# Kernel optimization log

Measured on AMD Instinct MI355X. Metric: run time of the kernel, lower is better.

The kernel has to match this reference:

```python
import jax, jax.numpy as jnp
import numpy as np

N_NODES = 100000
N_EDGES = 3200000


def setup_inputs() -> dict:
    key = jax.random.key(0)
    ks = jax.random.split(key, 8)
    n_in, h1, h2 = 512, 512, 128
    # xavier-uniform-ish scaling for weights
    lim1 = (6.0 / (n_in + h1)) ** 0.5
    lim2 = (6.0 / (h1 + h2)) ** 0.5
    return {
        "seq_a": jax.random.normal(ks[0], (N_NODES, n_in), dtype=jnp.float32),
        "W1": jax.random.uniform(ks[1], (n_in, h1), jnp.float32, -lim1, lim1),
        "b1": jnp.zeros((h1,), jnp.float32),
        "W2": jax.random.uniform(ks[2], (h1, h2), jnp.float32, -lim2, lim2),
        "b2": jnp.zeros((h2,), jnp.float32),
        "adj_rows": jnp.sort(jax.random.randint(ks[3], (N_EDGES,), 0, N_NODES, jnp.int32)),
        "adj_cols": jax.random.randint(ks[4], (N_EDGES,), 0, N_NODES, jnp.int32),
        "adj_vals": jax.random.uniform(ks[5], (N_EDGES,), jnp.float32),
    }


def reference(seq_a, W1, b1, W2, b2, adj_rows, adj_cols, adj_vals):
    # Eval-mode forward: F.dropout is identity when training=False.
    # MLP: Linear(n_in,512) + ReLU, Linear(512,128) (no activation on last layer)
    h = jax.nn.relu(seq_a @ W1 + b1)          # [N, 512]
    h_a = h @ W2 + b2                          # [N, 128]
    # Sparse aggregation: h_p = adj @ h_a with adj in COO form.
    # h_p[r] = sum over edges e with row r of vals[e] * h_a[cols[e]]
    msgs = adj_vals[:, None] * h_a[adj_cols]   # [E, 128] irregular gather
    h_p = jax.ops.segment_sum(msgs, adj_rows, num_segments=N_NODES)  # [N, 128]
    return (h_a, h_p)
```

## Files before the change

### kernel.cpp

```cpp
#include <hip/hip_runtime.h>

#define N_NODES 100000
#define ROWS_PAD 100096
#define NIN 512
#define H1  512
#define H2  128
#define N_EDGES 3200000

typedef __attribute__((ext_vector_type(8))) short bf16x8;
typedef __attribute__((ext_vector_type(4))) float f32x4;
typedef __attribute__((ext_vector_type(2))) float f32x2;

__device__ __forceinline__ unsigned short f2b(float x) {
  union { float f; unsigned int u; } c; c.f = x;
  unsigned int u = c.u;
  unsigned int r = (u + 0x7FFFu + ((u >> 16) & 1u)) >> 16;
  return (unsigned short)r;
}

typedef const __attribute__((address_space(1))) unsigned int* gp1_t;
typedef __attribute__((address_space(3))) unsigned int* sp3_t;
__device__ __forceinline__ void gl_lds16(const void* g, void* s) {
  __builtin_amdgcn_global_load_lds((gp1_t)g, (sp3_t)s, 16, 0, 0);
}

__device__ __forceinline__ unsigned cvtpk(float lo, float hi) {
  unsigned r;
  asm("v_cvt_pk_bf16_f32 %0, %1, %2" : "=v"(r) : "v"(lo), "v"(hi));
  return r;
}

__global__ void prep_w_kernel(const float* __restrict__ W1, const float* __restrict__ W2,
                              unsigned short* __restrict__ W1t, unsigned short* __restrict__ W2t) {
  int idx = blockIdx.x * blockDim.x + threadIdx.x;
  int stride = gridDim.x * blockDim.x;
  for (int i = idx; i < H1 * NIN; i += stride) {
    int n = i >> 9, k = i & 511;
    W1t[i] = f2b(W1[(size_t)(k ^ ((n & 7) << 3)) * H1 + n]);
  }
  for (int i = idx; i < H2 * H1; i += stride) {
    int n = i >> 9, k = i & 511;
    W2t[i] = f2b(W2[(size_t)(k ^ ((n & 7) << 3)) * H2 + n]);
  }
}

__global__ void rowptr_kernel(const int* __restrict__ rows, int* __restrict__ row_ptr) {
  int idx = blockIdx.x * blockDim.x + threadIdx.x;
  int stride = gridDim.x * blockDim.x;
  for (int e = idx; e < N_EDGES; e += stride) {
    int r = rows[e];
    int rp = (e == 0) ? -1 : rows[e - 1];
    for (int q = rp + 1; q <= r; ++q) row_ptr[q] = e;
  }
  int lastrow = rows[N_EDGES - 1];
  for (int q = idx; q <= N_NODES; q += stride)
    if (q > lastrow) row_ptr[q] = N_EDGES;
}

__global__ __launch_bounds__(256, 5) void gemm1_kernel(
    const float* __restrict__ A, const unsigned short* __restrict__ W1t,
    const float* __restrict__ b1, unsigned short* __restrict__ h_pre)
{
  __shared__ __align__(16) unsigned short SM[12288];
  const int tid = threadIdx.x;
  const int w = tid >> 6, lane = tid & 63;
  const int l15 = lane & 15, lg = lane >> 4;
  const int wr = w & 1, wc = w >> 1;
  const int hw = blockIdx.x;
  const int work = (hw & 7) * 782 + (hw >> 3);
  const int row0 = (work >> 2) << 6;
  const int n0 = (work & 3) << 7;

  int arow = row0 + (tid >> 2);
  if (arow > N_NODES - 1) arow = N_NODES - 1;
  const float* asrc = A + ((size_t)arow << 9) + ((tid & 3) << 4);
  const int alr  = tid >> 2;
  const int aswz = (alr & 7) << 4;
  const int ad0  = ((tid & 3) << 5);
  char* alds = (char*)SM + alr * 128;

  f32x4 acc[2][4];
  #pragma unroll
  for (int m = 0; m < 2; ++m)
    #pragma unroll
    for (int n = 0; n < 4; ++n) acc[m][n] = (f32x4){0.f, 0.f, 0.f, 0.f};

  const int so = tid * 16;

  f32x4 a0 = *(const f32x4*)(asrc);
  f32x4 a1 = *(const f32x4*)(asrc + 4);
  f32x4 a2 = *(const f32x4*)(asrc + 8);
  f32x4 a3 = *(const f32x4*)(asrc + 12);

  #pragma unroll
  for (int kt = 0; kt < 8; ++kt) {
    #pragma unroll
    for (int it = 0; it < 4; ++it) {
      int o = it * 4096 + so;
      int r = o >> 7, kb = o & 127;
      gl_lds16((const char*)W1t + (((size_t)(n0 + r)) << 10) + (kt << 7) + kb, (char*)SM + 8192 + o);
    }
    uint4 w0, w1;
    w0.x = cvtpk(a0[0], a0[1]); w0.y = cvtpk(a0[2], a0[3]);
    w0.z = cvtpk(a1[0], a1[1]); w0.w = cvtpk(a1[2], a1[3]);
    w1.x = cvtpk(a2[0], a2[1]); w1.y = cvtpk(a2[2], a2[3]);
    w1.z = cvtpk(a3[0], a3[1]); w1.w = cvtpk(a3[2], a3[3]);
    *(uint4*)(alds + ((ad0 +  0) ^ aswz)) = w0;
    *(uint4*)(alds + ((ad0 + 16) ^ aswz)) = w1;
    __builtin_amdgcn_sched_barrier(0);
    if (kt < 7) {
      const float* anp = asrc + ((kt + 1) << 6);
      a0 = *(const f32x4*)(anp);
      a1 = *(const f32x4*)(anp + 4);
      a2 = *(const f32x4*)(anp + 8);
      a3 = *(const f32x4*)(anp + 12);
      __builtin_amdgcn_sched_barrier(0);
      asm volatile("s_waitcnt vmcnt(4) lgkmcnt(0)" ::: "memory");
    } else {
      __builtin_amdgcn_sched_barrier(0);
      asm volatile("s_waitcnt vmcnt(0) lgkmcnt(0)" ::: "memory");
    }
    __builtin_amdgcn_s_barrier();
    __builtin_amdgcn_sched_barrier(0);
    #pragma unroll
    for (int ks = 0; ks < 2; ++ks) {
      bf16x8 af[2], bfr[4];
      #pragma unroll
      for (int m = 0; m < 2; ++m) {
        int r = wr * 32 + m * 16 + l15;
        af[m] = *(const bf16x8*)((const char*)SM + (r << 7) + (((ks << 6) + (lg << 4)) ^ ((r & 7) << 4)));
      }
      #pragma unroll
      for (int n = 0; n < 4; ++n) {
        int r = wc * 64 + n * 16 + l15;
        bfr[n] = *(const bf16x8*)((const char*)SM + 8192 + (r << 7) + (((ks << 6) + (lg << 4)) ^ ((r & 7) << 4)));
      }
      #pragma unroll
      for (int m = 0; m < 2; ++m)
        #pragma unroll
        for (int n = 0; n < 4; ++n)
          acc[m][n] = __builtin_amdgcn_mfma_f32_16x16x32_bf16(af[m], bfr[n], acc[m][n], 0, 0, 0);
    }
    __builtin_amdgcn_sched_barrier(0);
    __builtin_amdgcn_s_barrier();
  }

  #pragma unroll
  for (int n = 0; n < 4; ++n) {
    int cl = wc * 64 + n * 16 + l15;
    float bias = b1[n0 + cl];
    #pragma unroll
    for (int m = 0; m < 2; ++m) {
      #pragma unroll
      for (int q = 0; q < 4; ++q) {
        int rl = wr * 32 + m * 16 + lg * 4 + q;
        float v = acc[m][n][q] + bias;
        v = v > 0.f ? v : 0.f;
        SM[rl * 128 + (cl ^ ((rl & 7) << 3))] = f2b(v);
      }
    }
  }
  __syncthreads();
  #pragma unroll
  for (int p = 0; p < 4; ++p) {
    int ch = tid + p * 256;
    int row = ch >> 4, six = ch & 15;
    uint4 d = *(const uint4*)((const char*)SM + (ch << 4));
    *(uint4*)((char*)h_pre + (((size_t)(row0 + row)) << 10) + (n0 << 1) + (six << 4)) = d;
  }
}

__global__ __launch_bounds__(256, 5) void gemm2_kernel(
    const unsigned short* __restrict__ Hp, const unsigned short* __restrict__ W2t,
    const float* __restrict__ b2, float* __restrict__ ha_out, unsigned char* __restrict__ ha8)
{
  __shared__ __align__(16) unsigned short SM[12288];
  const int tid = threadIdx.x;
  const int w = tid >> 6, lane = tid & 63;
  const int l15 = lane & 15, lg = lane >> 4;
  const int wr = w & 1, wc = w >> 1;
  const int row0 = blockIdx.x << 6;

  f32x4 acc[2][4];
  #pragma unroll
  for (int m = 0; m < 2; ++m)
    #pragma unroll
    for (int n = 0; n < 4; ++n) acc[m][n] = (f32x4){0.f, 0.f, 0.f, 0.f};

  const int so = tid * 16;
  for (int kt = 0; kt < 8; ++kt) {
    #pragma unroll
    for (int it = 0; it < 2; ++it) {
      int o = it * 4096 + so;
      int r = o >> 7, kb = o & 127;
      gl_lds16((const char*)Hp + (((size_t)(row0 + r)) << 10) + (kt << 7) + kb, (char*)SM + o);
    }
    #pragma unroll
    for (int it = 0; it < 4; ++it) {
      int o = it * 4096 + so;
      int r = o >> 7, kb = o & 127;
      gl_lds16((const char*)W2t + (((size_t)r) << 10) + (kt << 7) + kb, (char*)SM + 8192 + o);
    }
    __syncthreads();
    #pragma unroll
    for (int ks = 0; ks < 2; ++ks) {
      bf16x8 af[2], bfr[4];
      #pragma unroll
      for (int m = 0; m < 2; ++m) {
        int r = wr * 32 + m * 16 + l15;
        af[m] = *(const bf16x8*)((const char*)SM + (r << 7) + (((ks << 6) + (lg << 4)) ^ ((r & 7) << 4)));
      }
      #pragma unroll
      for (int n = 0; n < 4; ++n) {
        int r = wc * 64 + n * 16 + l15;
        bfr[n] = *(const bf16x8*)((const char*)SM + 8192 + (r << 7) + (((ks << 6) + (lg << 4)) ^ ((r & 7) << 4)));
      }
      #pragma unroll
      for (int m = 0; m < 2; ++m)
        #pragma unroll
        for (int n = 0; n < 4; ++n)
          acc[m][n] = __builtin_amdgcn_mfma_f32_16x16x32_bf16(af[m], bfr[n], acc[m][n], 0, 0, 0);
    }
    __syncthreads();
  }

  #pragma unroll
  for (int n = 0; n < 4; ++n) {
    int col = wc * 64 + n * 16 + l15;
    float bias = b2[col];
    #pragma unroll
    for (int m = 0; m < 2; ++m) {
      #pragma unroll
      for (int q = 0; q < 4; ++q) {
        int row = row0 + wr * 32 + m * 16 + lg * 4 + q;
        if (row < N_NODES) {
          float v = acc[m][n][q] + bias;
          ha_out[((size_t)row << 7) + col] = v;
          int p8 = __builtin_amdgcn_cvt_pk_fp8_f32(v, v, 0, false);
          ha8[((size_t)row << 7) + col] = (unsigned char)(p8 & 0xff);
        }
      }
    }
  }
}

__global__ __launch_bounds__(256) void agg_csr_kernel(
    const int* __restrict__ row_ptr, const int* __restrict__ cols, const float* __restrict__ vals,
    const unsigned char* __restrict__ gtab8, float* __restrict__ hp)
{
  const int row = __builtin_amdgcn_readfirstlane((blockIdx.x * blockDim.x + threadIdx.x) >> 6);
  if (row >= N_NODES) return;
  const int lane = threadIdx.x & 63;
  const int e0 = row_ptr[row];
  const int e1 = row_ptr[row + 1];

  float acc0 = 0.f, acc1 = 0.f;
  int e = e0;
  for (; e + 8 <= e1; e += 8) {
    int c[8]; float v[8]; unsigned short g[8];
    #pragma unroll
    for (int j = 0; j < 8; ++j) { c[j] = cols[e + j]; v[j] = vals[e + j]; }
    #pragma unroll
    for (int j = 0; j < 8; ++j)
      g[j] = *(const unsigned short*)(gtab8 + ((size_t)c[j] << 7) + (lane << 1));
    float t0 = acc0, t1 = 0.f, u0 = acc1, u1 = 0.f;
    #pragma unroll
    for (int j = 0; j < 8; j += 2) {
      f32x2 f0 = __builtin_amdgcn_cvt_pk_f32_fp8((int)g[j+0], false);
      f32x2 f1 = __builtin_amdgcn_cvt_pk_f32_fp8((int)g[j+1], false);
      t0 = fmaf(v[j+0], f0.x, t0);
      t1 = fmaf(v[j+1], f1.x, t1);
      u0 = fmaf(v[j+0], f0.y, u0);
      u1 = fmaf(v[j+1], f1.y, u1);
    }
    acc0 = t0 + t1; acc1 = u0 + u1;
  }
  for (; e < e1; ++e) {
    int c = cols[e];
    float v = vals[e];
    unsigned short g = *(const unsigned short*)(gtab8 + ((size_t)c << 7) + (lane << 1));
    f32x2 f = __builtin_amdgcn_cvt_pk_f32_fp8((int)g, false);
    acc0 = fmaf(v, f.x, acc0);
    acc1 = fmaf(v, f.y, acc1);
  }
  float2 st; st.x = acc0; st.y = acc1;
  *(float2*)&hp[((size_t)row << 7) + (lane << 1)] = st;
}

extern "C" void kernel_launch(void* const* d_in, const int* in_sizes, int n_in,
                              void* d_out, int out_size, void* d_ws, size_t ws_size,
                              hipStream_t stream) {
  const float* seq_a    = (const float*)d_in[0];
  const float* W1       = (const float*)d_in[1];
  const float* b1       = (const float*)d_in[2];
  const float* W2       = (const float*)d_in[3];
  const float* b2       = (const float*)d_in[4];
  const int*   adj_rows = (const int*)d_in[5];
  const int*   adj_cols = (const int*)d_in[6];
  const float* adj_vals = (const float*)d_in[7];

  unsigned short* h_pre = (unsigned short*)d_ws;
  unsigned short* W1t   = h_pre + (size_t)ROWS_PAD * H1;
  unsigned short* W2t   = W1t + (size_t)H1 * NIN;
  unsigned char*  ha8   = (unsigned char*)(W2t + (size_t)H2 * H1);
  int*            row_ptr = (int*)(ha8 + (size_t)N_NODES * H2);

  float* ha_out = (float*)d_out;
  float* hp     = ha_out + (size_t)N_NODES * H2;

  prep_w_kernel<<<1280, 256, 0, stream>>>(W1, W2, W1t, W2t);
  rowptr_kernel<<<2048, 256, 0, stream>>>(adj_rows, row_ptr);
  gemm1_kernel<<<6256, 256, 0, stream>>>(seq_a, W1t, b1, h_pre);
  gemm2_kernel<<<1564, 256, 0, stream>>>(h_pre, W2t, b2, ha_out, ha8);
  agg_csr_kernel<<<(ROWS_PAD * 64) / 256, 256, 0, stream>>>(row_ptr, adj_cols, adj_vals, ha8, hp);
}
```

Baseline: 259.1 us.

## Fuse both MLP GEMMs into one kernel and merge prep kernels

Merges gemm1 and gemm2 into a single kernel. Each 64-row block loops over four 128-column chunks of the hidden layer, applies bias and ReLU, keeps the bf16 result in LDS and immediately accumulates it into the 128-wide output using W2t fragments loaded straight from global memory. This removes the bf16 hidden-activation buffer and its full write and read through HBM. The weight-transpose and row-pointer kernels are also combined into one launch. In exchange, each block re-reads its fp32 input tile once per chunk, uses more LDS with lower occupancy, and the grid has a quarter as many blocks.

```diff
diff --git a/kernel.cpp b/kernel.cpp
--- a/kernel.cpp
+++ b/kernel.cpp
@@ -30,8 +30,10 @@
   return r;
 }
 
-__global__ void prep_w_kernel(const float* __restrict__ W1, const float* __restrict__ W2,
-                              unsigned short* __restrict__ W1t, unsigned short* __restrict__ W2t) {
+__global__ void prep_kernel(const float* __restrict__ W1, const float* __restrict__ W2,
+                            const int* __restrict__ rows,
+                            unsigned short* __restrict__ W1t, unsigned short* __restrict__ W2t,
+                            int* __restrict__ row_ptr) {
   int idx = blockIdx.x * blockDim.x + threadIdx.x;
   int stride = gridDim.x * blockDim.x;
   for (int i = idx; i < H1 * NIN; i += stride) {
@@ -42,11 +44,6 @@
     int n = i >> 9, k = i & 511;
     W2t[i] = f2b(W2[(size_t)(k ^ ((n & 7) << 3)) * H2 + n]);
   }
-}
-
-__global__ void rowptr_kernel(const int* __restrict__ rows, int* __restrict__ row_ptr) {
-  int idx = blockIdx.x * blockDim.x + threadIdx.x;
-  int stride = gridDim.x * blockDim.x;
   for (int e = idx; e < N_EDGES; e += stride) {
     int r = rows[e];
     int rp = (e == 0) ? -1 : rows[e - 1];
@@ -57,19 +54,17 @@
     if (q > lastrow) row_ptr[q] = N_EDGES;
 }
 
-__global__ __launch_bounds__(256, 5) void gemm1_kernel(
+__global__ __launch_bounds__(256, 4) void mlp_kernel(
     const float* __restrict__ A, const unsigned short* __restrict__ W1t,
-    const float* __restrict__ b1, unsigned short* __restrict__ h_pre)
+    const unsigned short* __restrict__ W2t, const float* __restrict__ b1,
+    const float* __restrict__ b2, float* __restrict__ ha_out, unsigned char* __restrict__ ha8)
 {
-  __shared__ __align__(16) unsigned short SM[12288];
+  __shared__ __align__(16) unsigned short SM[20480];
   const int tid = threadIdx.x;
   const int w = tid >> 6, lane = tid & 63;
   const int l15 = lane & 15, lg = lane >> 4;
   const int wr = w & 1, wc = w >> 1;
-  const int hw = blockIdx.x;
-  const int work = (hw & 7) * 782 + (hw >> 3);
-  const int row0 = (work >> 2) << 6;
-  const int n0 = (work & 3) << 7;
+  const int row0 = blockIdx.x << 6;
 
   int arow = row0 + (tid >> 2);
   if (arow > N_NODES - 1) arow = N_NODES - 1;
@@ -79,154 +74,125 @@
   const int ad0  = ((tid & 3) << 5);
   char* alds = (char*)SM + alr * 128;
 
-  f32x4 acc[2][4];
+  const int so = tid * 16;
+
+  f32x4 acc_ha[2][4];
   #pragma unroll
   for (int m = 0; m < 2; ++m)
     #pragma unroll
-    for (int n = 0; n < 4; ++n) acc[m][n] = (f32x4){0.f, 0.f, 0.f, 0.f};
-
-  const int so = tid * 16;
-
-  f32x4 a0 = *(const f32x4*)(asrc);
-  f32x4 a1 = *(const f32x4*)(asrc + 4);
-  f32x4 a2 = *(const f32x4*)(asrc + 8);
-  f32x4 a3 = *(const f32x4*)(asrc + 12);
-
-  #pragma unroll
-  for (int kt = 0; kt < 8; ++kt) {
-    #pragma unroll
-    for (int it = 0; it < 4; ++it) {
-      int o = it * 4096 + so;
-      int r = o >> 7, kb = o & 127;
-      gl_lds16((const char*)W1t + (((size_t)(n0 + r)) << 10) + (kt << 7) + kb, (char*)SM + 8192 + o);
-    }
-    uint4 w0, w1;
-    w0.x = cvtpk(a0[0], a0[1]); w0.y = cvtpk(a0[2], a0[3]);
-    w0.z = cvtpk(a1[0], a1[1]); w0.w = cvtpk(a1[2], a1[3]);
-    w1.x = cvtpk(a2[0], a2[1]); w1.y = cvtpk(a2[2], a2[3]);
-    w1.z = cvtpk(a3[0], a3[1]); w1.w = cvtpk(a3[2], a3[3]);
-    *(uint4*)(alds + ((ad0 +  0) ^ aswz)) = w0;
-    *(uint4*)(alds + ((ad0 + 16) ^ aswz)) = w1;
-    __builtin_amdgcn_sched_barrier(0);
-    if (kt < 7) {
-      const float* anp = asrc + ((kt + 1) << 6);
-      a0 = *(const f32x4*)(anp);
-      a1 = *(const f32x4*)(anp + 4);
-      a2 = *(const f32x4*)(anp + 8);
-      a3 = *(const f32x4*)(anp + 12);
+    for (int n = 0; n < 4; ++n) acc_ha[m][n] = (f32x4){0.f, 0.f, 0.f, 0.f};
+
+  #pragma unroll 1
+  for (int nc = 0; nc < 4; ++nc) {
+    f32x4 a0 = *(const f32x4*)(asrc);
+    f32x4 a1 = *(const f32x4*)(asrc + 4);
+    f32x4 a2 = *(const f32x4*)(asrc + 8);
+    f32x4 a3 = *(const f32x4*)(asrc + 12);
+
+    f32x4 accT[2][4];
+    #pragma unroll
+    for (int m = 0; m < 2; ++m)
+      #pragma unroll
+      for (int n = 0; n < 4; ++n) accT[m][n] = (f32x4){0.f, 0.f, 0.f, 0.f};
+
+    #pragma unroll
+    for (int kt = 0; kt < 8; ++kt) {
+      #pragma unroll
+      for (int it = 0; it < 4; ++it) {
+        int o = it * 4096 + so;
+        int r = o >> 7, kb = o & 127;
+        gl_lds16((const char*)W1t + (((size_t)((nc << 7) + r)) << 10) + (kt << 7) + kb,
+                 (char*)SM + 8192 + o);
+      }
+      uint4 w0, w1;
+      w0.x = cvtpk(a0[0], a0[1]); w0.y = cvtpk(a0[2], a0[3]);
+      w0.z = cvtpk(a1[0], a1[1]); w0.w = cvtpk(a1[2], a1[3]);
+      w1.x = cvtpk(a2[0], a2[1]); w1.y = cvtpk(a2[2], a2[3]);
+      w1.z = cvtpk(a3[0], a3[1]); w1.w = cvtpk(a3[2], a3[3]);
+      *(uint4*)(alds + ((ad0 +  0) ^ aswz)) = w0;
+      *(uint4*)(alds + ((ad0 + 16) ^ aswz)) = w1;
       __builtin_amdgcn_sched_barrier(0);
-      asm volatile("s_waitcnt vmcnt(4) lgkmcnt(0)" ::: "memory");
-    } else {
+      if (kt < 7) {
+        const float* anp = asrc + ((kt + 1) << 6);
+        a0 = *(const f32x4*)(anp);
+        a1 = *(const f32x4*)(anp + 4);
+        a2 = *(const f32x4*)(anp + 8);
+        a3 = *(const f32x4*)(anp + 12);
+        __builtin_amdgcn_sched_barrier(0);
+        asm volatile("s_waitcnt vmcnt(4) lgkmcnt(0)" ::: "memory");
+      } else {
+        __builtin_amdgcn_sched_barrier(0);
+        asm volatile("s_waitcnt vmcnt(0) lgkmcnt(0)" ::: "memory");
+      }
+      __builtin_amdgcn_s_barrier();
       __builtin_amdgcn_sched_barrier(0);
-      asm volatile("s_waitcnt vmcnt(0) lgkmcnt(0)" ::: "memory");
-    }
-    __builtin_amdgcn_s_barrier();
-    __builtin_amdgcn_sched_barrier(0);
-    #pragma unroll
-    for (int ks = 0; ks < 2; ++ks) {
-      bf16x8 af[2], bfr[4];
+      #pragma unroll
+      for (int ks = 0; ks < 2; ++ks) {
+        bf16x8 af[2], bfr[4];
+        #pragma unroll
+        for (int m = 0; m < 2; ++m) {
+          int r = wr * 32 + m * 16 + l15;
+          af[m] = *(const bf16x8*)((const char*)SM + (r << 7) + (((ks << 6) + (lg << 4)) ^ ((r & 7) << 4)));
+        }
+        #pragma unroll
+        for (int n = 0; n < 4; ++n) {
+          int r = wc * 64 + n * 16 + l15;
+          bfr[n] = *(const bf16x8*)((const char*)SM + 8192 + (r << 7) + (((ks << 6) + (lg << 4)) ^ ((r & 7) << 4)));
+        }
+        #pragma unroll
+        for (int m = 0; m < 2; ++m)
+          #pragma unroll
+          for (int n = 0; n < 4; ++n)
+            accT[m][n] = __builtin_amdgcn_mfma_f32_16x16x32_bf16(af[m], bfr[n], accT[m][n], 0, 0, 0);
+      }
+      __builtin_amdgcn_sched_barrier(0);
+      __builtin_amdgcn_s_barrier();
+    }
+
+    #pragma unroll
+    for (int n = 0; n < 4; ++n) {
+      int cl = wc * 64 + n * 16 + l15;
+      float bias = b1[(nc << 7) + cl];
+      #pragma unroll
+      for (int m = 0; m < 2; ++m) {
+        #pragma unroll
+        for (int q = 0; q < 4; ++q) {
+          int rl = wr * 32 + m * 16 + lg * 4 + q;
+          float v = accT[m][n][q] + bias;
+          v = v > 0.f ? v : 0.f;
+          *(unsigned short*)((char*)SM + 24576 + rl * 256 + (((cl << 1)) ^ ((rl & 7) << 4))) = f2b(v);
+        }
+      }
+    }
+    __syncthreads();
+
+    #pragma unroll
+    for (int kk = 0; kk < 4; ++kk) {
+      bf16x8 bw[4];
+      #pragma unroll
+      for (int nf = 0; nf < 4; ++nf) {
+        int n = wc * 64 + nf * 16 + l15;
+        int kl = (nc << 7) + (kk << 5) + (lg << 3);
+        bw[nf] = *(const bf16x8*)(W2t + ((size_t)n << 9) + (kl ^ ((n & 7) << 3)));
+      }
+      bf16x8 af[2];
       #pragma unroll
       for (int m = 0; m < 2; ++m) {
         int r = wr * 32 + m * 16 + l15;
-        af[m] = *(const bf16x8*)((const char*)SM + (r << 7) + (((ks << 6) + (lg << 4)) ^ ((r & 7) << 4)));
-      }
-      #pragma unroll
-      for (int n = 0; n < 4; ++n) {
-        int r = wc * 64 + n * 16 + l15;
-        bfr[n] = *(const bf16x8*)((const char*)SM + 8192 + (r << 7) + (((ks << 6) + (lg << 4)) ^ ((r & 7) << 4)));
+        af[m] = *(const bf16x8*)((const char*)SM + 24576 + (r << 8) + (((kk << 6) + (lg << 4)) ^ ((r & 7) << 4)));
       }
       #pragma unroll
       for (int m = 0; m < 2; ++m)
         #pragma unroll
-        for (int n = 0; n < 4; ++n)
-          acc[m][n] = __builtin_amdgcn_mfma_f32_16x16x32_bf16(af[m], bfr[n], acc[m][n], 0, 0, 0);
-    }
-    __builtin_amdgcn_sched_barrier(0);
-    __builtin_amdgcn_s_barrier();
+        for (int nf = 0; nf < 4; ++nf)
+          acc_ha[m][nf] = __builtin_amdgcn_mfma_f32_16x16x32_bf16(af[m], bw[nf], acc_ha[m][nf], 0, 0, 0);
+    }
+    __syncthreads();
   }
 
   #pragma unroll
-  for (int n = 0; n < 4; ++n) {
-    int cl = wc * 64 + n * 16 + l15;
-    float bias = b1[n0 + cl];
-    #pragma unroll
-    for (int m = 0; m < 2; ++m) {
-      #pragma unroll
-      for (int q = 0; q < 4; ++q) {
-        int rl = wr * 32 + m * 16 + lg * 4 + q;
-        float v = acc[m][n][q] + bias;
-        v = v > 0.f ? v : 0.f;
-        SM[rl * 128 + (cl ^ ((rl & 7) << 3))] = f2b(v);
-      }
-    }
-  }
-  __syncthreads();
-  #pragma unroll
-  for (int p = 0; p < 4; ++p) {
-    int ch = tid + p * 256;
-    int row = ch >> 4, six = ch & 15;
-    uint4 d = *(const uint4*)((const char*)SM + (ch << 4));
-    *(uint4*)((char*)h_pre + (((size_t)(row0 + row)) << 10) + (n0 << 1) + (six << 4)) = d;
-  }
-}
-
-__global__ __launch_bounds__(256, 5) void gemm2_kernel(
-    const unsigned short* __restrict__ Hp, const unsigned short* __restrict__ W2t,
-    const float* __restrict__ b2, float* __restrict__ ha_out, unsigned char* __restrict__ ha8)
-{
-  __shared__ __align__(16) unsigned short SM[12288];
-  const int tid = threadIdx.x;
-  const int w = tid >> 6, lane = tid & 63;
-  const int l15 = lane & 15, lg = lane >> 4;
-  const int wr = w & 1, wc = w >> 1;
-  const int row0 = blockIdx.x << 6;
-
-  f32x4 acc[2][4];
-  #pragma unroll
-  for (int m = 0; m < 2; ++m)
-    #pragma unroll
-    for (int n = 0; n < 4; ++n) acc[m][n] = (f32x4){0.f, 0.f, 0.f, 0.f};
-
-  const int so = tid * 16;
-  for (int kt = 0; kt < 8; ++kt) {
-    #pragma unroll
-    for (int it = 0; it < 2; ++it) {
-      int o = it * 4096 + so;
-      int r = o >> 7, kb = o & 127;
-      gl_lds16((const char*)Hp + (((size_t)(row0 + r)) << 10) + (kt << 7) + kb, (char*)SM + o);
-    }
-    #pragma unroll
-    for (int it = 0; it < 4; ++it) {
-      int o = it * 4096 + so;
-      int r = o >> 7, kb = o & 127;
-      gl_lds16((const char*)W2t + (((size_t)r) << 10) + (kt << 7) + kb, (char*)SM + 8192 + o);
-    }
-    __syncthreads();
-    #pragma unroll
-    for (int ks = 0; ks < 2; ++ks) {
-      bf16x8 af[2], bfr[4];
-      #pragma unroll
-      for (int m = 0; m < 2; ++m) {
-        int r = wr * 32 + m * 16 + l15;
-        af[m] = *(const bf16x8*)((const char*)SM + (r << 7) + (((ks << 6) + (lg << 4)) ^ ((r & 7) << 4)));
-      }
-      #pragma unroll
-      for (int n = 0; n < 4; ++n) {
-        int r = wc * 64 + n * 16 + l15;
-        bfr[n] = *(const bf16x8*)((const char*)SM + 8192 + (r << 7) + (((ks << 6) + (lg << 4)) ^ ((r & 7) << 4)));
-      }
-      #pragma unroll
-      for (int m = 0; m < 2; ++m)
-        #pragma unroll
-        for (int n = 0; n < 4; ++n)
-          acc[m][n] = __builtin_amdgcn_mfma_f32_16x16x32_bf16(af[m], bfr[n], acc[m][n], 0, 0, 0);
-    }
-    __syncthreads();
-  }
-
-  #pragma unroll
-  for (int n = 0; n < 4; ++n) {
-    int col = wc * 64 + n * 16 + l15;
+  for (int nf = 0; nf < 4; ++nf) {
+    int col = wc * 64 + nf * 16 + l15;
     float bias = b2[col];
     #pragma unroll
     for (int m = 0; m < 2; ++m) {
@@ -234,7 +200,7 @@
       for (int q = 0; q < 4; ++q) {
         int row = row0 + wr * 32 + m * 16 + lg * 4 + q;
         if (row < N_NODES) {
-          float v = acc[m][n][q] + bias;
+          float v = acc_ha[m][nf][q] + bias;
           ha_out[((size_t)row << 7) + col] = v;
           int p8 = __builtin_amdgcn_cvt_pk_fp8_f32(v, v, 0, false);
           ha8[((size_t)row << 7) + col] = (unsigned char)(p8 & 0xff);
@@ -299,8 +265,7 @@
   const int*   adj_cols = (const int*)d_in[6];
   const float* adj_vals = (const float*)d_in[7];
 
-  unsigned short* h_pre = (unsigned short*)d_ws;
-  unsigned short* W1t   = h_pre + (size_t)ROWS_PAD * H1;
+  unsigned short* W1t   = (unsigned short*)d_ws;
   unsigned short* W2t   = W1t + (size_t)H1 * NIN;
   unsigned char*  ha8   = (unsigned char*)(W2t + (size_t)H2 * H1);
   int*            row_ptr = (int*)(ha8 + (size_t)N_NODES * H2);
@@ -308,9 +273,7 @@
   float* ha_out = (float*)d_out;
   float* hp     = ha_out + (size_t)N_NODES * H2;
 
-  prep_w_kernel<<<1280, 256, 0, stream>>>(W1, W2, W1t, W2t);
-  rowptr_kernel<<<2048, 256, 0, stream>>>(adj_rows, row_ptr);
-  gemm1_kernel<<<6256, 256, 0, stream>>>(seq_a, W1t, b1, h_pre);
-  gemm2_kernel<<<1564, 256, 0, stream>>>(h_pre, W2t, b2, ha_out, ha8);
+  prep_kernel<<<2048, 256, 0, stream>>>(W1, W2, adj_rows, W1t, W2t, row_ptr);
+  mlp_kernel<<<ROWS_PAD / 64, 256, 0, stream>>>(seq_a, W1t, W2t, b1, b2, ha_out, ha8);
   agg_csr_kernel<<<(ROWS_PAD * 64) / 256, 256, 0, stream>>>(row_ptr, adj_cols, adj_vals, ha8, hp);
 }
```

Measured after the change: 390.2 us. 1.51x slower.
